# Kernel optimization log

Hardware: AMD Instinct MI355X
Metric: run time of the kernel (lower is better)

The kernel has to match this reference:

```python
import jax, jax.numpy as jnp
import numpy as np

HOURS = 24
ALPHA, BETA, GAMMA, DELTA = 1.0, 2.0, 1.0, 0.5
TEMP = 0.1
WIN = 2  # window_size in _peak_shape_loss
NEG = -1e9

B, S = 16384, 1440  # 60 days of hourly data


def setup_inputs() -> dict:
    key = jax.random.key(0)
    k1, k2 = jax.random.split(key)
    y_pred = jax.random.normal(k1, (B, S), dtype=jnp.float32)
    y_true = jax.random.normal(k2, (B, S), dtype=jnp.float32)
    # default daytime mask from the module: hour in [6, 20]
    hours = jnp.tile(jnp.arange(HOURS), S // HOURS)  # (S,)
    day = ((hours >= 6) & (hours <= 20)).astype(jnp.float32)
    is_daytime = jnp.broadcast_to(day, (B, S))
    return {"y_pred": y_pred, "y_true": y_true, "is_daytime": is_daytime}


def _soft_peaks(y, day_mask):
    # y, day_mask: (B, D, H) -> soft peak values/times per day: (B, D)
    masked = jnp.where(day_mask > 0.5, y, NEG)
    attn = jax.nn.softmax(masked / TEMP, axis=-1)
    vals = jnp.sum(attn * y, axis=-1)
    t = jnp.arange(HOURS, dtype=y.dtype)
    times = jnp.sum(attn * t, axis=-1)
    return vals, times


def reference(y_pred, y_true, is_daytime):
    b, s = y_true.shape
    d = s // HOURS
    yp = y_pred[:, : d * HOURS].reshape(b, d, HOURS)
    yt = y_true[:, : d * HOURS].reshape(b, d, HOURS)
    dm = is_daytime[:, : d * HOURS].reshape(b, d, HOURS)

    L_overall = jnp.mean((y_pred - y_true) ** 2)

    tv, tt = _soft_peaks(yt, dm)
    pv, pt = _soft_peaks(yp, dm)
    L_mag = jnp.mean((pv - tv) ** 2)
    L_time = jnp.mean((pt - tt) ** 2)

    masked_true = jnp.where(dm > 0.5, yt, NEG)
    peak = jnp.argmax(masked_true, axis=-1)  # (B, D) int
    offs = jnp.arange(-WIN, WIN + 1)
    idx = peak[..., None] + offs  # (B, D, 5)
    valid = (idx >= 0) & (idx < HOURS)  # emulates window clipping at day edges
    idx_c = jnp.clip(idx, 0, HOURS - 1)
    tw = jnp.take_along_axis(yt, idx_c, axis=-1)  # (B, D, 5)
    pw = jnp.take_along_axis(yp, idx_c, axis=-1)
    vmask = valid.astype(yt.dtype)
    cnt = jnp.sum(vmask, axis=-1)  # window length per (B, D)
    tmax = jnp.max(jnp.where(valid, tw, -jnp.inf), axis=-1, keepdims=True)
    pmax = jnp.max(jnp.where(valid, pw, -jnp.inf), axis=-1, keepdims=True)
    tn = tw / (tmax + 1e-6)
    pn = pw / (pmax + 1e-6)
    per = jnp.sum((pn - tn) ** 2 * vmask, axis=-1) / cnt  # per-window MSE
    L_shape = jnp.sum(per) / (b * d + 1e-6)

    return ALPHA * L_overall + BETA * L_mag + GAMMA * L_time + DELTA * L_shape
```

## Files before the change

### kernel.cpp

```cpp
#include <hip/hip_runtime.h>
#include <math.h>


#define HOURS_ 24
#define WIN_ 2
#define NEGV (-1e9f)

__global__ __launch_bounds__(256) void splloss_days(
    const float* __restrict__ ypred,
    const float* __restrict__ ytrue,
    const float* __restrict__ isday,
    float4* __restrict__ partials,
    int n_days)
{
    int g = blockIdx.x * 256 + threadIdx.x;
    float o = 0.f, mg = 0.f, tl = 0.f, sh = 0.f;

    if (g < n_days) {
        float a[HOURS_];
        float b[HOURS_];
        unsigned dmask = 0u;
        const float4* p4 = reinterpret_cast<const float4*>(ypred + (size_t)g * HOURS_);
        const float4* t4 = reinterpret_cast<const float4*>(ytrue + (size_t)g * HOURS_);
        const float4* d4 = reinterpret_cast<const float4*>(isday + (size_t)g * HOURS_);
        #pragma unroll
        for (int k = 0; k < 6; ++k) {
            float4 vp = p4[k];
            float4 vt = t4[k];
            float4 vd = d4[k];
            a[4*k+0] = vp.x; a[4*k+1] = vp.y; a[4*k+2] = vp.z; a[4*k+3] = vp.w;
            b[4*k+0] = vt.x; b[4*k+1] = vt.y; b[4*k+2] = vt.z; b[4*k+3] = vt.w;
            dmask |= (vd.x > 0.5f ? 1u : 0u) << (4*k+0);
            dmask |= (vd.y > 0.5f ? 1u : 0u) << (4*k+1);
            dmask |= (vd.z > 0.5f ? 1u : 0u) << (4*k+2);
            dmask |= (vd.w > 0.5f ? 1u : 0u) << (4*k+3);
        }

        #pragma unroll
        for (int h = 0; h < HOURS_; ++h) { float d = a[h] - b[h]; o += d * d; }

        float mt = -INFINITY, mp = -INFINITY;
        int peak = 0;
        #pragma unroll
        for (int h = 0; h < HOURS_; ++h) {
            bool day = (dmask >> h) & 1u;
            float bm = day ? b[h] : NEGV;
            float am = day ? a[h] : NEGV;
            if (bm > mt) { mt = bm; peak = h; }
            mp = fmaxf(mp, am);
        }

        float set = 0.f, syt = 0.f, sht = 0.f;
        float sep = 0.f, syp = 0.f, shp = 0.f;
        #pragma unroll
        for (int h = 0; h < HOURS_; ++h) {
            bool day = (dmask >> h) & 1u;
            float bm = day ? b[h] : NEGV;
            float am = day ? a[h] : NEGV;
            float et = __expf((bm - mt) * 10.f);
            float ep = __expf((am - mp) * 10.f);
            set += et; syt += et * b[h]; sht += et * (float)h;
            sep += ep; syp += ep * a[h]; shp += ep * (float)h;
        }
        float tv = syt / set, tt = sht / set;
        float pv = syp / sep, pt = shp / sep;
        mg = (pv - tv) * (pv - tv);
        tl = (pt - tt) * (pt - tt);

        float tw[5], pw[5];
        bool  val[5];
        float tmax = -INFINITY, pmax = -INFINITY, cnt = 0.f;
        #pragma unroll
        for (int j = 0; j < 5; ++j) {
            int idx = peak + j - WIN_;
            bool v = (idx >= 0) && (idx < HOURS_);
            int ic = idx < 0 ? 0 : (idx > HOURS_ - 1 ? HOURS_ - 1 : idx);
            float tg = b[0], pg = a[0];
            #pragma unroll
            for (int h = 1; h < HOURS_; ++h) {
                bool e = (ic == h);
                tg = e ? b[h] : tg;
                pg = e ? a[h] : pg;
            }
            tw[j] = tg; pw[j] = pg; val[j] = v;
            if (v) { tmax = fmaxf(tmax, tg); pmax = fmaxf(pmax, pg); cnt += 1.f; }
        }
        float rt = 1.f / (tmax + 1e-6f);
        float rp = 1.f / (pmax + 1e-6f);
        float ss = 0.f;
        #pragma unroll
        for (int j = 0; j < 5; ++j) {
            float tn = tw[j] * rt, pn = pw[j] * rp;
            float d = pn - tn;
            ss += val[j] ? d * d : 0.f;
        }
        sh = ss / cnt;
    }

    #pragma unroll
    for (int off = 32; off > 0; off >>= 1) {
        o  += __shfl_down(o,  off);
        mg += __shfl_down(mg, off);
        tl += __shfl_down(tl, off);
        sh += __shfl_down(sh, off);
    }
    __shared__ float4 red[4];
    int wid = threadIdx.x >> 6;
    if ((threadIdx.x & 63) == 0) red[wid] = make_float4(o, mg, tl, sh);
    __syncthreads();
    if (threadIdx.x == 0) {
        float4 r0 = red[0], r1 = red[1], r2 = red[2], r3 = red[3];
        partials[blockIdx.x] = make_float4(r0.x + r1.x + r2.x + r3.x,
                                           r0.y + r1.y + r2.y + r3.y,
                                           r0.z + r1.z + r2.z + r3.z,
                                           r0.w + r1.w + r2.w + r3.w);
    }
}

__global__ __launch_bounds__(256) void splloss_final(
    const float4* __restrict__ partials, int nb, float* __restrict__ out,
    double inv_bs, double inv_bd, double inv_shape)
{
    double o = 0.0, m = 0.0, t = 0.0, s = 0.0;
    for (int i = threadIdx.x; i < nb; i += 256) {
        float4 p = partials[i];
        o += (double)p.x; m += (double)p.y; t += (double)p.z; s += (double)p.w;
    }
    #pragma unroll
    for (int off = 32; off > 0; off >>= 1) {
        o += __shfl_down(o, off);
        m += __shfl_down(m, off);
        t += __shfl_down(t, off);
        s += __shfl_down(s, off);
    }
    __shared__ double red[4][4];
    int wid = threadIdx.x >> 6;
    if ((threadIdx.x & 63) == 0) { red[wid][0] = o; red[wid][1] = m; red[wid][2] = t; red[wid][3] = s; }
    __syncthreads();
    if (threadIdx.x == 0) {
        double ot = red[0][0] + red[1][0] + red[2][0] + red[3][0];
        double mt = red[0][1] + red[1][1] + red[2][1] + red[3][1];
        double tt = red[0][2] + red[1][2] + red[2][2] + red[3][2];
        double st = red[0][3] + red[1][3] + red[2][3] + red[3][3];
        double total = 1.0 * (ot * inv_bs)
                     + 2.0 * (mt * inv_bd)
                     + 1.0 * (tt * inv_bd)
                     + 0.5 * (st * inv_shape);
        out[0] = (float)total;
    }
}

extern "C" void kernel_launch(void* const* d_in, const int* in_sizes, int n_in,
                              void* d_out, int out_size, void* d_ws, size_t ws_size,
                              hipStream_t stream) {
    const float* yp = (const float*)d_in[0];
    const float* yt = (const float*)d_in[1];
    const float* dm = (const float*)d_in[2];
    float* out = (float*)d_out;

    int n = in_sizes[0];
    int n_days = n / HOURS_;
    int nb = (n_days + 255) / 256;

    float4* partials = (float4*)d_ws;

    splloss_days<<<nb, 256, 0, stream>>>(yp, yt, dm, partials, n_days);

    double inv_bs    = 1.0 / (double)n;
    double inv_bd    = 1.0 / (double)n_days;
    double inv_shape = 1.0 / ((double)n_days + 1e-6);
    splloss_final<<<1, 256, 0, stream>>>(partials, nb, out, inv_bs, inv_bd, inv_shape);
}
```

Baseline: 268.0 us.

## Stage day data through transposed LDS for coalesced loads and indexed window gather

Each block now loads its 256 days cooperatively with consecutive float4 chunks per thread, which coalesces the global reads, then transposes them into padded shared memory so each thread reads its own day's 24 hours. The daytime mask is built in LDS with atomicOr. The peak-window gather now indexes shared memory directly instead of running a 24-way select chain. The cost is about 49KB of LDS per block, which limits occupancy, plus two barriers and LDS atomics.

```diff
diff --git a/kernel.cpp b/kernel.cpp
--- a/kernel.cpp
+++ b/kernel.cpp
@@ -5,6 +5,8 @@
 #define HOURS_ 24
 #define WIN_ 2
 #define NEGV (-1e9f)
+#define DPB 256
+#define LDP (DPB + 1)
 
 __global__ __launch_bounds__(256) void splloss_days(
     const float* __restrict__ ypred,
@@ -13,36 +15,60 @@
     float4* __restrict__ partials,
     int n_days)
 {
-    int g = blockIdx.x * 256 + threadIdx.x;
+    __shared__ float apT[HOURS_][LDP];
+    __shared__ float atT[HOURS_][LDP];
+    __shared__ unsigned maskLds[DPB];
+
+    const int tid  = threadIdx.x;
+    const int day0 = blockIdx.x * DPB;
+    const int vdays = min(DPB, n_days - day0);
+    const int vchunks = vdays * 6;
+
+    const float4* p4 = reinterpret_cast<const float4*>(ypred) + (size_t)day0 * 6;
+    const float4* t4 = reinterpret_cast<const float4*>(ytrue) + (size_t)day0 * 6;
+    const float4* d4 = reinterpret_cast<const float4*>(isday) + (size_t)day0 * 6;
+    float4 vp[6], vt[6], vd[6];
+    #pragma unroll
+    for (int j = 0; j < 6; ++j) {
+        int c = tid + j * 256;
+        if (c < vchunks) { vp[j] = p4[c]; vt[j] = t4[c]; vd[j] = d4[c]; }
+    }
+
+    maskLds[tid] = 0u;
+    __syncthreads();
+
+    #pragma unroll
+    for (int j = 0; j < 6; ++j) {
+        int c = tid + j * 256;
+        if (c < vchunks) {
+            int day = c / 6;
+            int h0  = (c - day * 6) * 4;
+            apT[h0 + 0][day] = vp[j].x; apT[h0 + 1][day] = vp[j].y;
+            apT[h0 + 2][day] = vp[j].z; apT[h0 + 3][day] = vp[j].w;
+            atT[h0 + 0][day] = vt[j].x; atT[h0 + 1][day] = vt[j].y;
+            atT[h0 + 2][day] = vt[j].z; atT[h0 + 3][day] = vt[j].w;
+            unsigned bits = (vd[j].x > 0.5f ? 1u : 0u)
+                          | (vd[j].y > 0.5f ? 2u : 0u)
+                          | (vd[j].z > 0.5f ? 4u : 0u)
+                          | (vd[j].w > 0.5f ? 8u : 0u);
+            atomicOr(&maskLds[day], bits << h0);
+        }
+    }
+    __syncthreads();
+
     float o = 0.f, mg = 0.f, tl = 0.f, sh = 0.f;
-
-    if (g < n_days) {
-        float a[HOURS_];
-        float b[HOURS_];
-        unsigned dmask = 0u;
-        const float4* p4 = reinterpret_cast<const float4*>(ypred + (size_t)g * HOURS_);
-        const float4* t4 = reinterpret_cast<const float4*>(ytrue + (size_t)g * HOURS_);
-        const float4* d4 = reinterpret_cast<const float4*>(isday + (size_t)g * HOURS_);
+    if (tid < vdays) {
+        unsigned dmask = maskLds[tid];
+        float a[HOURS_], b[HOURS_];
         #pragma unroll
-        for (int k = 0; k < 6; ++k) {
-            float4 vp = p4[k];
-            float4 vt = t4[k];
-            float4 vd = d4[k];
-            a[4*k+0] = vp.x; a[4*k+1] = vp.y; a[4*k+2] = vp.z; a[4*k+3] = vp.w;
-            b[4*k+0] = vt.x; b[4*k+1] = vt.y; b[4*k+2] = vt.z; b[4*k+3] = vt.w;
-            dmask |= (vd.x > 0.5f ? 1u : 0u) << (4*k+0);
-            dmask |= (vd.y > 0.5f ? 1u : 0u) << (4*k+1);
-            dmask |= (vd.z > 0.5f ? 1u : 0u) << (4*k+2);
-            dmask |= (vd.w > 0.5f ? 1u : 0u) << (4*k+3);
-        }
-
-        #pragma unroll
-        for (int h = 0; h < HOURS_; ++h) { float d = a[h] - b[h]; o += d * d; }
+        for (int h = 0; h < HOURS_; ++h) { a[h] = apT[h][tid]; b[h] = atT[h][tid]; }
 
         float mt = -INFINITY, mp = -INFINITY;
         int peak = 0;
         #pragma unroll
         for (int h = 0; h < HOURS_; ++h) {
+            float d = a[h] - b[h];
+            o += d * d;
             bool day = (dmask >> h) & 1u;
             float bm = day ? b[h] : NEGV;
             float am = day ? a[h] : NEGV;
@@ -68,20 +94,15 @@
         tl = (pt - tt) * (pt - tt);
 
         float tw[5], pw[5];
-        bool  val[5];
         float tmax = -INFINITY, pmax = -INFINITY, cnt = 0.f;
+        bool val[5];
         #pragma unroll
         for (int j = 0; j < 5; ++j) {
             int idx = peak + j - WIN_;
             bool v = (idx >= 0) && (idx < HOURS_);
             int ic = idx < 0 ? 0 : (idx > HOURS_ - 1 ? HOURS_ - 1 : idx);
-            float tg = b[0], pg = a[0];
-            #pragma unroll
-            for (int h = 1; h < HOURS_; ++h) {
-                bool e = (ic == h);
-                tg = e ? b[h] : tg;
-                pg = e ? a[h] : pg;
-            }
+            float tg = atT[ic][tid];
+            float pg = apT[ic][tid];
             tw[j] = tg; pw[j] = pg; val[j] = v;
             if (v) { tmax = fmaxf(tmax, tg); pmax = fmaxf(pmax, pg); cnt += 1.f; }
         }
@@ -160,7 +181,7 @@
 
     int n = in_sizes[0];
     int n_days = n / HOURS_;
-    int nb = (n_days + 255) / 256;
+    int nb = (n_days + DPB - 1) / DPB;
 
     float4* partials = (float4*)d_ws;
 
```

Measured after the change: 274.4 us. +2.4%, slower.

## Split each day across two lanes with shuffle merges and grid-stride loop

Applied to the files above, without the earlier changes.

Each day is now processed by a pair of threads, each holding 12 hours, and partial max, argmax, softmax sums and window max are combined with xor shuffles. The peak window is computed with range masks instead of a 24-way select gather. The launch switches to a capped grid of 1920 blocks with a grid-stride loop over days. This aims to cut per-thread register use and serial work and to make the loads more coalesced, at the cost of extra shuffles and duplicated per-day work across the two lanes.

```diff
diff --git a/kernel.cpp b/kernel.cpp
--- a/kernel.cpp
+++ b/kernel.cpp
@@ -13,88 +13,105 @@
     float4* __restrict__ partials,
     int n_days)
 {
-    int g = blockIdx.x * 256 + threadIdx.x;
+    const int tid  = threadIdx.x;
+    const int half = tid & 1;
+    const int h0g  = half * 12;
+    const int dayStride = (gridDim.x * 256) >> 1;
+
     float o = 0.f, mg = 0.f, tl = 0.f, sh = 0.f;
 
-    if (g < n_days) {
-        float a[HOURS_];
-        float b[HOURS_];
-        unsigned dmask = 0u;
-        const float4* p4 = reinterpret_cast<const float4*>(ypred + (size_t)g * HOURS_);
-        const float4* t4 = reinterpret_cast<const float4*>(ytrue + (size_t)g * HOURS_);
-        const float4* d4 = reinterpret_cast<const float4*>(isday + (size_t)g * HOURS_);
-        #pragma unroll
-        for (int k = 0; k < 6; ++k) {
-            float4 vp = p4[k];
-            float4 vt = t4[k];
-            float4 vd = d4[k];
-            a[4*k+0] = vp.x; a[4*k+1] = vp.y; a[4*k+2] = vp.z; a[4*k+3] = vp.w;
-            b[4*k+0] = vt.x; b[4*k+1] = vt.y; b[4*k+2] = vt.z; b[4*k+3] = vt.w;
-            dmask |= (vd.x > 0.5f ? 1u : 0u) << (4*k+0);
-            dmask |= (vd.y > 0.5f ? 1u : 0u) << (4*k+1);
-            dmask |= (vd.z > 0.5f ? 1u : 0u) << (4*k+2);
-            dmask |= (vd.w > 0.5f ? 1u : 0u) << (4*k+3);
-        }
+    for (int day = (blockIdx.x * 256 + tid) >> 1; day < n_days; day += dayStride) {
+        const float4* p4 = reinterpret_cast<const float4*>(ypred + (size_t)day * 24 + h0g);
+        const float4* t4 = reinterpret_cast<const float4*>(ytrue + (size_t)day * 24 + h0g);
+        const float4* d4 = reinterpret_cast<const float4*>(isday + (size_t)day * 24 + h0g);
+        float4 pa0 = p4[0], pa1 = p4[1], pa2 = p4[2];
+        float4 ta0 = t4[0], ta1 = t4[1], ta2 = t4[2];
+        float4 da0 = d4[0], da1 = d4[1], da2 = d4[2];
+
+        float a[12] = {pa0.x, pa0.y, pa0.z, pa0.w, pa1.x, pa1.y, pa1.z, pa1.w,
+                       pa2.x, pa2.y, pa2.z, pa2.w};
+        float b[12] = {ta0.x, ta0.y, ta0.z, ta0.w, ta1.x, ta1.y, ta1.z, ta1.w,
+                       ta2.x, ta2.y, ta2.z, ta2.w};
+        float dm[12] = {da0.x, da0.y, da0.z, da0.w, da1.x, da1.y, da1.z, da1.w,
+                        da2.x, da2.y, da2.z, da2.w};
 
         #pragma unroll
-        for (int h = 0; h < HOURS_; ++h) { float d = a[h] - b[h]; o += d * d; }
+        for (int k = 0; k < 12; ++k) { float d = a[k] - b[k]; o += d * d; }
 
         float mt = -INFINITY, mp = -INFINITY;
-        int peak = 0;
+        int pk = h0g;
         #pragma unroll
-        for (int h = 0; h < HOURS_; ++h) {
-            bool day = (dmask >> h) & 1u;
-            float bm = day ? b[h] : NEGV;
-            float am = day ? a[h] : NEGV;
-            if (bm > mt) { mt = bm; peak = h; }
+        for (int k = 0; k < 12; ++k) {
+            bool dy = dm[k] > 0.5f;
+            float bm = dy ? b[k] : NEGV;
+            float am = dy ? a[k] : NEGV;
+            if (bm > mt) { mt = bm; pk = h0g + k; }
             mp = fmaxf(mp, am);
+        }
+        {
+            float mt_o = __shfl_xor(mt, 1);
+            int   pk_o = __shfl_xor(pk, 1);
+            float mp_o = __shfl_xor(mp, 1);
+            bool takeo = (mt_o > mt) || (mt_o == mt && pk_o < pk);
+            pk = takeo ? pk_o : pk;
+            mt = fmaxf(mt, mt_o);
+            mp = fmaxf(mp, mp_o);
         }
 
         float set = 0.f, syt = 0.f, sht = 0.f;
         float sep = 0.f, syp = 0.f, shp = 0.f;
         #pragma unroll
-        for (int h = 0; h < HOURS_; ++h) {
-            bool day = (dmask >> h) & 1u;
-            float bm = day ? b[h] : NEGV;
-            float am = day ? a[h] : NEGV;
+        for (int k = 0; k < 12; ++k) {
+            bool dy = dm[k] > 0.5f;
+            float bm = dy ? b[k] : NEGV;
+            float am = dy ? a[k] : NEGV;
             float et = __expf((bm - mt) * 10.f);
             float ep = __expf((am - mp) * 10.f);
-            set += et; syt += et * b[h]; sht += et * (float)h;
-            sep += ep; syp += ep * a[h]; shp += ep * (float)h;
+            float hh = (float)(h0g + k);
+            set += et; syt += et * b[k]; sht += et * hh;
+            sep += ep; syp += ep * a[k]; shp += ep * hh;
         }
-        float tv = syt / set, tt = sht / set;
-        float pv = syp / sep, pt = shp / sep;
-        mg = (pv - tv) * (pv - tv);
-        tl = (pt - tt) * (pt - tt);
+        set += __shfl_xor(set, 1);
+        syt += __shfl_xor(syt, 1);
+        sht += __shfl_xor(sht, 1);
+        sep += __shfl_xor(sep, 1);
+        syp += __shfl_xor(syp, 1);
+        shp += __shfl_xor(shp, 1);
+        {
+            float tv = syt / set, tt = sht / set;
+            float pv = syp / sep, pt = shp / sep;
+            float dmg = (pv - tv) * (pv - tv);
+            float dtl = (pt - tt) * (pt - tt);
+            mg += half ? 0.f : dmg;
+            tl += half ? 0.f : dtl;
+        }
 
-        float tw[5], pw[5];
-        bool  val[5];
-        float tmax = -INFINITY, pmax = -INFINITY, cnt = 0.f;
+        int lo = pk - WIN_; if (lo < 0) lo = 0;
+        int hi = pk + WIN_; if (hi > 23) hi = 23;
+        float cnt = (float)(hi - lo + 1);
+        float twmax = -INFINITY, pwmax = -INFINITY;
         #pragma unroll
-        for (int j = 0; j < 5; ++j) {
-            int idx = peak + j - WIN_;
-            bool v = (idx >= 0) && (idx < HOURS_);
-            int ic = idx < 0 ? 0 : (idx > HOURS_ - 1 ? HOURS_ - 1 : idx);
-            float tg = b[0], pg = a[0];
+        for (int k = 0; k < 12; ++k) {
+            int hg = h0g + k;
+            bool in = (hg >= lo) && (hg <= hi);
+            twmax = in ? fmaxf(twmax, b[k]) : twmax;
+            pwmax = in ? fmaxf(pwmax, a[k]) : pwmax;
+        }
+        twmax = fmaxf(twmax, __shfl_xor(twmax, 1));
+        pwmax = fmaxf(pwmax, __shfl_xor(pwmax, 1));
+        {
+            float rt = 1.f / (twmax + 1e-6f);
+            float rp = 1.f / (pwmax + 1e-6f);
+            float ss = 0.f;
             #pragma unroll
-            for (int h = 1; h < HOURS_; ++h) {
-                bool e = (ic == h);
-                tg = e ? b[h] : tg;
-                pg = e ? a[h] : pg;
+            for (int k = 0; k < 12; ++k) {
+                int hg = h0g + k;
+                bool in = (hg >= lo) && (hg <= hi);
+                float d = a[k] * rp - b[k] * rt;
+                ss += in ? d * d : 0.f;
             }
-            tw[j] = tg; pw[j] = pg; val[j] = v;
-            if (v) { tmax = fmaxf(tmax, tg); pmax = fmaxf(pmax, pg); cnt += 1.f; }
+            sh += ss / cnt;
         }
-        float rt = 1.f / (tmax + 1e-6f);
-        float rp = 1.f / (pmax + 1e-6f);
-        float ss = 0.f;
-        #pragma unroll
-        for (int j = 0; j < 5; ++j) {
-            float tn = tw[j] * rt, pn = pw[j] * rp;
-            float d = pn - tn;
-            ss += val[j] ? d * d : 0.f;
-        }
-        sh = ss / cnt;
     }
 
     #pragma unroll
@@ -160,7 +177,10 @@
 
     int n = in_sizes[0];
     int n_days = n / HOURS_;
-    int nb = (n_days + 255) / 256;
+
+    int nb = 1920;
+    int nbMax = (n_days + 127) / 128;
+    if (nbMax < nb) nb = nbMax;
 
     float4* partials = (float4*)d_ws;
 
```

Result: no change. 268.3 us (+0.1%).

## Split each day across four lanes with DPP reductions and prefetching grid-stride loop

Applied to the files above, without the earlier changes.

Each day is now handled by four lanes, each owning six hours, and per-day maxima, argmax and softmax sums are combined across the lanes with DPP cross-lane ops. A persistent grid-stride loop preloads the next day's data while computing the current one. This targets poor coalescing and the high register pressure of the one-thread-per-day layout. In exchange it adds cross-lane shuffle overhead and tie-breaking logic for argmax.

```diff
diff --git a/kernel.cpp b/kernel.cpp
--- a/kernel.cpp
+++ b/kernel.cpp
@@ -6,95 +6,171 @@
 #define WIN_ 2
 #define NEGV (-1e9f)
 
-__global__ __launch_bounds__(256) void splloss_days(
+__device__ __forceinline__ float frcp(float x) { return __builtin_amdgcn_rcpf(x); }
+
+#define DPP_XOR1 0xB1
+#define DPP_XOR2 0x4E
+
+template<int CTRL>
+__device__ __forceinline__ int dpp_i(int src) {
+    return __builtin_amdgcn_update_dpp(0, src, CTRL, 0xF, 0xF, true);
+}
+template<int CTRL>
+__device__ __forceinline__ float dpp_f(float x) {
+    return __int_as_float(dpp_i<CTRL>(__float_as_int(x)));
+}
+
+__device__ __forceinline__ void seg_body(
+    float2 p0, float2 p1, float2 p2,
+    float2 t0, float2 t1, float2 t2,
+    float2 m0, float2 m1, float2 m2,
+    int seg, float vfl,
+    float& o, float& mg, float& tl, float& sh)
+{
+    const int h0 = seg * 6;
+    float a[6]  = {p0.x, p0.y, p1.x, p1.y, p2.x, p2.y};
+    float b[6]  = {t0.x, t0.y, t1.x, t1.y, t2.x, t2.y};
+    float dm[6] = {m0.x, m0.y, m1.x, m1.y, m2.x, m2.y};
+
+    float oo = 0.f;
+    #pragma unroll
+    for (int k = 0; k < 6; ++k) { float d = a[k] - b[k]; oo = fmaf(d, d, oo); }
+    o = fmaf(oo, vfl, o);
+
+    float bm[6], am[6];
+    #pragma unroll
+    for (int k = 0; k < 6; ++k) {
+        bool dy = dm[k] > 0.5f;
+        bm[k] = dy ? b[k] : NEGV;
+        am[k] = dy ? a[k] : NEGV;
+    }
+
+    bool  s0 = bm[1] > bm[0]; float v01 = s0 ? bm[1] : bm[0]; int i01 = s0 ? h0+1 : h0;
+    bool  s1 = bm[3] > bm[2]; float v23 = s1 ? bm[3] : bm[2]; int i23 = s1 ? h0+3 : h0+2;
+    bool  s2 = bm[5] > bm[4]; float v45 = s2 ? bm[5] : bm[4]; int i45 = s2 ? h0+5 : h0+4;
+    bool  tA = v23 > v01; float mt = tA ? v23 : v01; int pk = tA ? i23 : i01;
+    bool  tB = v45 > mt;  mt = tB ? v45 : mt;        pk = tB ? i45 : pk;
+    float mp = fmaxf(fmaxf(fmaxf(am[0], am[1]), fmaxf(am[2], am[3])),
+                     fmaxf(am[4], am[5]));
+
+    {
+        float mt_o = dpp_f<DPP_XOR1>(mt); int pk_o = dpp_i<DPP_XOR1>(pk);
+        float mp_o = dpp_f<DPP_XOR1>(mp);
+        bool to = (mt_o > mt) || (mt_o == mt && pk_o < pk);
+        pk = to ? pk_o : pk; mt = fmaxf(mt, mt_o); mp = fmaxf(mp, mp_o);
+        mt_o = dpp_f<DPP_XOR2>(mt); pk_o = dpp_i<DPP_XOR2>(pk);
+        mp_o = dpp_f<DPP_XOR2>(mp);
+        to = (mt_o > mt) || (mt_o == mt && pk_o < pk);
+        pk = to ? pk_o : pk; mt = fmaxf(mt, mt_o); mp = fmaxf(mp, mp_o);
+    }
+
+    float mt10 = mt * 10.f, mp10 = mp * 10.f;
+    float set = 0.f, syt = 0.f, sht = 0.f;
+    float sep = 0.f, syp = 0.f, shp = 0.f;
+    #pragma unroll
+    for (int k = 0; k < 6; ++k) {
+        float et = __expf(fmaf(bm[k], 10.f, -mt10));
+        float ep = __expf(fmaf(am[k], 10.f, -mp10));
+        float hh = (float)(h0 + k);
+        set += et; syt = fmaf(et, b[k], syt); sht = fmaf(et, hh, sht);
+        sep += ep; syp = fmaf(ep, a[k], syp); shp = fmaf(ep, hh, shp);
+    }
+    set += dpp_f<DPP_XOR1>(set); set += dpp_f<DPP_XOR2>(set);
+    syt += dpp_f<DPP_XOR1>(syt); syt += dpp_f<DPP_XOR2>(syt);
+    sht += dpp_f<DPP_XOR1>(sht); sht += dpp_f<DPP_XOR2>(sht);
+    sep += dpp_f<DPP_XOR1>(sep); sep += dpp_f<DPP_XOR2>(sep);
+    syp += dpp_f<DPP_XOR1>(syp); syp += dpp_f<DPP_XOR2>(syp);
+    shp += dpp_f<DPP_XOR1>(shp); shp += dpp_f<DPP_XOR2>(shp);
+    {
+        float rs = frcp(set), rq = frcp(sep);
+        float d1 = syp * rq - syt * rs;
+        float d2 = shp * rq - sht * rs;
+        float once = (seg == 0) ? vfl : 0.f;
+        mg = fmaf(d1 * d1, once, mg);
+        tl = fmaf(d2 * d2, once, tl);
+    }
+
+    int lo = pk - WIN_; lo = lo < 0 ? 0 : lo;
+    int hi = pk + WIN_; hi = hi > 23 ? 23 : hi;
+    int cnt = hi - lo + 1;
+    float invcnt = (cnt == 5) ? 0.2f : ((cnt == 4) ? 0.25f : (1.f / 3.f));
+    float twm = -INFINITY, pwm = -INFINITY;
+    #pragma unroll
+    for (int k = 0; k < 6; ++k) {
+        int hg = h0 + k;
+        bool in = (hg >= lo) && (hg <= hi);
+        twm = in ? fmaxf(twm, b[k]) : twm;
+        pwm = in ? fmaxf(pwm, a[k]) : pwm;
+    }
+    twm = fmaxf(twm, dpp_f<DPP_XOR1>(twm)); twm = fmaxf(twm, dpp_f<DPP_XOR2>(twm));
+    pwm = fmaxf(pwm, dpp_f<DPP_XOR1>(pwm)); pwm = fmaxf(pwm, dpp_f<DPP_XOR2>(pwm));
+    {
+        float rt = frcp(twm + 1e-6f);
+        float rp = frcp(pwm + 1e-6f);
+        float ss = 0.f;
+        #pragma unroll
+        for (int k = 0; k < 6; ++k) {
+            int hg = h0 + k;
+            bool in = (hg >= lo) && (hg <= hi);
+            float d = fmaf(a[k], rp, -(b[k] * rt));
+            ss = in ? fmaf(d, d, ss) : ss;
+        }
+        sh = fmaf(ss * invcnt, vfl, sh);
+    }
+}
+
+__global__ __launch_bounds__(256, 6) void splloss_days(
     const float* __restrict__ ypred,
     const float* __restrict__ ytrue,
     const float* __restrict__ isday,
     float4* __restrict__ partials,
-    int n_days)
+    int n_days, int nit)
 {
-    int g = blockIdx.x * 256 + threadIdx.x;
+    const int tid = threadIdx.x;
+    const int seg = tid & 3;
+    const int grp = tid >> 2;
+    const int dayStride = gridDim.x * 64;
+    int day = blockIdx.x * 64 + grp;
+
+    const int segOff = seg * 6;
+
     float o = 0.f, mg = 0.f, tl = 0.f, sh = 0.f;
 
-    if (g < n_days) {
-        float a[HOURS_];
-        float b[HOURS_];
-        unsigned dmask = 0u;
-        const float4* p4 = reinterpret_cast<const float4*>(ypred + (size_t)g * HOURS_);
-        const float4* t4 = reinterpret_cast<const float4*>(ytrue + (size_t)g * HOURS_);
-        const float4* d4 = reinterpret_cast<const float4*>(isday + (size_t)g * HOURS_);
-        #pragma unroll
-        for (int k = 0; k < 6; ++k) {
-            float4 vp = p4[k];
-            float4 vt = t4[k];
-            float4 vd = d4[k];
-            a[4*k+0] = vp.x; a[4*k+1] = vp.y; a[4*k+2] = vp.z; a[4*k+3] = vp.w;
-            b[4*k+0] = vt.x; b[4*k+1] = vt.y; b[4*k+2] = vt.z; b[4*k+3] = vt.w;
-            dmask |= (vd.x > 0.5f ? 1u : 0u) << (4*k+0);
-            dmask |= (vd.y > 0.5f ? 1u : 0u) << (4*k+1);
-            dmask |= (vd.z > 0.5f ? 1u : 0u) << (4*k+2);
-            dmask |= (vd.w > 0.5f ? 1u : 0u) << (4*k+3);
-        }
-
-        #pragma unroll
-        for (int h = 0; h < HOURS_; ++h) { float d = a[h] - b[h]; o += d * d; }
-
-        float mt = -INFINITY, mp = -INFINITY;
-        int peak = 0;
-        #pragma unroll
-        for (int h = 0; h < HOURS_; ++h) {
-            bool day = (dmask >> h) & 1u;
-            float bm = day ? b[h] : NEGV;
-            float am = day ? a[h] : NEGV;
-            if (bm > mt) { mt = bm; peak = h; }
-            mp = fmaxf(mp, am);
-        }
-
-        float set = 0.f, syt = 0.f, sht = 0.f;
-        float sep = 0.f, syp = 0.f, shp = 0.f;
-        #pragma unroll
-        for (int h = 0; h < HOURS_; ++h) {
-            bool day = (dmask >> h) & 1u;
-            float bm = day ? b[h] : NEGV;
-            float am = day ? a[h] : NEGV;
-            float et = __expf((bm - mt) * 10.f);
-            float ep = __expf((am - mp) * 10.f);
-            set += et; syt += et * b[h]; sht += et * (float)h;
-            sep += ep; syp += ep * a[h]; shp += ep * (float)h;
-        }
-        float tv = syt / set, tt = sht / set;
-        float pv = syp / sep, pt = shp / sep;
-        mg = (pv - tv) * (pv - tv);
-        tl = (pt - tt) * (pt - tt);
-
-        float tw[5], pw[5];
-        bool  val[5];
-        float tmax = -INFINITY, pmax = -INFINITY, cnt = 0.f;
-        #pragma unroll
-        for (int j = 0; j < 5; ++j) {
-            int idx = peak + j - WIN_;
-            bool v = (idx >= 0) && (idx < HOURS_);
-            int ic = idx < 0 ? 0 : (idx > HOURS_ - 1 ? HOURS_ - 1 : idx);
-            float tg = b[0], pg = a[0];
-            #pragma unroll
-            for (int h = 1; h < HOURS_; ++h) {
-                bool e = (ic == h);
-                tg = e ? b[h] : tg;
-                pg = e ? a[h] : pg;
-            }
-            tw[j] = tg; pw[j] = pg; val[j] = v;
-            if (v) { tmax = fmaxf(tmax, tg); pmax = fmaxf(pmax, pg); cnt += 1.f; }
-        }
-        float rt = 1.f / (tmax + 1e-6f);
-        float rp = 1.f / (pmax + 1e-6f);
-        float ss = 0.f;
-        #pragma unroll
-        for (int j = 0; j < 5; ++j) {
-            float tn = tw[j] * rt, pn = pw[j] * rp;
-            float d = pn - tn;
-            ss += val[j] ? d * d : 0.f;
-        }
-        sh = ss / cnt;
+    int   dA = day < n_days ? day : 0;
+    float vA = day < n_days ? 1.f : 0.f;
+    const float2* pA = reinterpret_cast<const float2*>(ypred + (size_t)dA * 24 + segOff);
+    const float2* tA = reinterpret_cast<const float2*>(ytrue + (size_t)dA * 24 + segOff);
+    const float2* mA = reinterpret_cast<const float2*>(isday + (size_t)dA * 24 + segOff);
+    float2 a0 = pA[0], a1 = pA[1], a2 = pA[2];
+    float2 b0 = tA[0], b1 = tA[1], b2 = tA[2];
+    float2 c0 = mA[0], c1 = mA[1], c2 = mA[2];
+
+    for (int it = 0; it < nit; it += 2) {
+        int   day1 = day + dayStride;
+        int   dB = day1 < n_days ? day1 : 0;
+        float vB = day1 < n_days ? 1.f : 0.f;
+        const float2* pB = reinterpret_cast<const float2*>(ypred + (size_t)dB * 24 + segOff);
+        const float2* tB = reinterpret_cast<const float2*>(ytrue + (size_t)dB * 24 + segOff);
+        const float2* mB = reinterpret_cast<const float2*>(isday + (size_t)dB * 24 + segOff);
+        float2 e0 = pB[0], e1 = pB[1], e2 = pB[2];
+        float2 f0 = tB[0], f1 = tB[1], f2 = tB[2];
+        float2 g0 = mB[0], g1 = mB[1], g2 = mB[2];
+
+        seg_body(a0, a1, a2, b0, b1, b2, c0, c1, c2, seg, vA, o, mg, tl, sh);
+
+        int   day2 = day + 2 * dayStride;
+        int   dC = day2 < n_days ? day2 : 0;
+        vA = day2 < n_days ? 1.f : 0.f;
+        const float2* pC = reinterpret_cast<const float2*>(ypred + (size_t)dC * 24 + segOff);
+        const float2* tC = reinterpret_cast<const float2*>(ytrue + (size_t)dC * 24 + segOff);
+        const float2* mC = reinterpret_cast<const float2*>(isday + (size_t)dC * 24 + segOff);
+        a0 = pC[0]; a1 = pC[1]; a2 = pC[2];
+        b0 = tC[0]; b1 = tC[1]; b2 = tC[2];
+        c0 = mC[0]; c1 = mC[1]; c2 = mC[2];
+
+        seg_body(e0, e1, e2, f0, f1, f2, g0, g1, g2, seg, vB, o, mg, tl, sh);
+
+        day = day2;
     }
 
     #pragma unroll
@@ -160,11 +236,15 @@
 
     int n = in_sizes[0];
     int n_days = n / HOURS_;
-    int nb = (n_days + 255) / 256;
+
+    int nb = (n_days + 63) / 64;
+    if (nb > 1536) nb = 1536;
+    int perIter = nb * 64;
+    int nit = (n_days + perIter - 1) / perIter;
 
     float4* partials = (float4*)d_ws;
 
-    splloss_days<<<nb, 256, 0, stream>>>(yp, yt, dm, partials, n_days);
+    splloss_days<<<nb, 256, 0, stream>>>(yp, yt, dm, partials, n_days, nit);
 
     double inv_bs    = 1.0 / (double)n;
     double inv_bd    = 1.0 / (double)n_days;
```

New measurement: 283.4 us. 5.7% more time.
